# Kernel optimization log

Hardware: AMD Instinct MI355X
Metric: run time of the kernel (lower is better)

Reference implementation:

```python
import jax, jax.numpy as jnp
import numpy as np

DIM = 1024
D_STATE = 16
D_CONV = 4
EXPAND = 2
D_INNER = EXPAND * DIM          # 2048
DT_RANK = DIM // 16             # 64 (ceil(1024/16))
BATCH = 4096
LN_EPS = 1e-5


def setup_inputs() -> dict:
    key = jax.random.key(0)
    ks = jax.random.split(key, 8)
    s = lambda k, shape, sc=0.02: (jax.random.normal(k, shape, jnp.float32) * sc)
    return {
        "x": jax.random.normal(ks[0], (BATCH, DIM), jnp.float32),
        "ln_gamma": jnp.ones((DIM,), jnp.float32),
        "ln_beta": jnp.zeros((DIM,), jnp.float32),
        "W_in": s(ks[1], (2 * D_INNER, DIM)),            # in_proj (no bias)
        "conv_w": s(ks[2], (D_INNER, D_CONV), 0.2),      # depthwise causal conv
        "conv_b": jnp.zeros((D_INNER,), jnp.float32),
        "W_xproj": s(ks[3], (DT_RANK + 2 * D_STATE, D_INNER)),
        "W_dt": s(ks[4], (D_INNER, DT_RANK), 0.1),
        "b_dt": s(ks[5], (D_INNER,), 0.5),
        "A_log": jnp.log(jnp.broadcast_to(
            jnp.arange(1, D_STATE + 1, dtype=jnp.float32), (D_INNER, D_STATE))),
        "Dskip": jnp.ones((D_INNER,), jnp.float32),
        "W_out": s(ks[6], (DIM, D_INNER)),               # out_proj (no bias)
    }


def _mamba_layer(x, ln_gamma, ln_beta, W_in, conv_w, conv_b,
                 W_xproj, W_dt, b_dt, A_log, Dskip, W_out):
    # x: [B, dim] -> unsqueeze(1): [B, L=1, dim]
    xs = x[:, None, :]
    # LayerNorm over last dim
    mu = jnp.mean(xs, axis=-1, keepdims=True)
    var = jnp.var(xs, axis=-1, keepdims=True)
    xn = (xs - mu) * jax.lax.rsqrt(var + LN_EPS) * ln_gamma + ln_beta
    # in_proj -> split into x, z   [B, L, d_inner] each
    xz = jnp.einsum('bld,ed->ble', xn, W_in)
    xi, z = jnp.split(xz, 2, axis=-1)
    L = xi.shape[1]
    # depthwise causal conv1d (kernel d_conv, left pad d_conv-1)
    xp = jnp.pad(xi, ((0, 0), (D_CONV - 1, 0), (0, 0)))
    xc = conv_b + sum(conv_w[:, k] * xp[:, k:k + L, :] for k in range(D_CONV))
    xc = jax.nn.silu(xc)
    # x_proj -> dt, B, C
    xdb = jnp.einsum('bld,ed->ble', xc, W_xproj)
    dt, Bm, Cm = jnp.split(xdb, [DT_RANK, DT_RANK + D_STATE], axis=-1)
    dt = jax.nn.softplus(jnp.einsum('blr,dr->bld', dt, W_dt) + b_dt)  # [B,L,d_inner]
    A = -jnp.exp(A_log)                                              # [d_inner,d_state]
    dA = jnp.exp(dt[..., None] * A)                                  # [B,L,d_inner,d_state]
    dBu = dt[..., None] * Bm[:, :, None, :] * xc[..., None]          # [B,L,d_inner,d_state]

    def step(h, inp):
        dA_l, dBu_l, C_l = inp
        h = dA_l * h + dBu_l                    # [B,d_inner,d_state]
        y = jnp.einsum('bdn,bn->bd', h, C_l)    # [B,d_inner]
        return h, y

    h0 = jnp.zeros((x.shape[0], D_INNER, D_STATE), x.dtype)
    _, ys = jax.lax.scan(step, h0, (dA.swapaxes(0, 1), dBu.swapaxes(0, 1), Cm.swapaxes(0, 1)))
    y = ys.swapaxes(0, 1) + Dskip * xc          # [B,L,d_inner]
    y = y * jax.nn.silu(z)
    out = jnp.einsum('ble,de->bld', y, W_out)   # [B,L,dim]
    return out[:, 0, :]                          # squeeze(1)


def reference(x, ln_gamma, ln_beta, W_in, conv_w, conv_b,
              W_xproj, W_dt, b_dt, A_log, Dskip, W_out):
    return _mamba_layer(x, ln_gamma, ln_beta, W_in, conv_w, conv_b,
                        W_xproj, W_dt, b_dt, A_log, Dskip, W_out)
```

## Files before the change

### kernel.cpp

```cpp
#include <hip/hip_runtime.h>
#include <hip/hip_bf16.h>
#include <stdint.h>

#define DIM     1024
#define DINNER  2048
#define BATCH   4096
#define LN_EPS  1e-5f

typedef unsigned short u16;
using f32x4  = __attribute__((ext_vector_type(4))) float;
using bf16x8 = __attribute__((ext_vector_type(8))) __bf16;

__device__ __forceinline__ float bf2f(u16 h) {
    union { unsigned u; float f; } v; v.u = ((unsigned)h) << 16; return v.f;
}
__device__ __forceinline__ u16 f2bf(float f) {
    union { float f; unsigned u; } v; v.f = f;
    unsigned r = v.u + 0x7fffu + ((v.u >> 16) & 1u);
    return (u16)(r >> 16);
}
__device__ __forceinline__ float silu_f(float x) {
    return x / (1.f + __expf(-x));
}

#define AS1 __attribute__((address_space(1)))
#define AS3 __attribute__((address_space(3)))

__device__ __forceinline__ unsigned lds_u32(const void* p) {
    return (unsigned)(unsigned long long)(const AS3 void*)p;
}

__global__ __launch_bounds__(256)
void cvt_ln(const float* __restrict__ x, const float* __restrict__ gamma,
            const float* __restrict__ beta, u16* __restrict__ xn,
            const float4* __restrict__ s0, ushort4* __restrict__ d0, int n0,
            const float4* __restrict__ s1, ushort4* __restrict__ d1, int n1,
            const float4* __restrict__ s2, ushort4* __restrict__ d2, int n2,
            const float4* __restrict__ s3, ushort4* __restrict__ d3, int n3)
{
    const int t = threadIdx.x;
    if (blockIdx.x < BATCH) {
        const int row = blockIdx.x;
        float4 v = ((const float4*)(x + (size_t)row * DIM))[t];
        float s1v = v.x + v.y + v.z + v.w;
        float s2v = v.x*v.x + v.y*v.y + v.z*v.z + v.w*v.w;
        #pragma unroll
        for (int o = 32; o > 0; o >>= 1) {
            s1v += __shfl_down(s1v, o);
            s2v += __shfl_down(s2v, o);
        }
        __shared__ float red[8];
        __shared__ float mv[2];
        const int w = t >> 6, l = t & 63;
        if (l == 0) { red[w] = s1v; red[4 + w] = s2v; }
        __syncthreads();
        if (t == 0) {
            float a = red[0] + red[1] + red[2] + red[3];
            float b = red[4] + red[5] + red[6] + red[7];
            float mu = a * (1.f / DIM);
            float var = b * (1.f / DIM) - mu * mu;
            mv[0] = mu; mv[1] = rsqrtf(var + LN_EPS);
        }
        __syncthreads();
        const float mu = mv[0], rs = mv[1];
        float4 g  = ((const float4*)gamma)[t];
        float4 be = ((const float4*)beta)[t];
        ushort4 o = make_ushort4(
            f2bf((v.x - mu) * rs * g.x + be.x),
            f2bf((v.y - mu) * rs * g.y + be.y),
            f2bf((v.z - mu) * rs * g.z + be.z),
            f2bf((v.w - mu) * rs * g.w + be.w));
        *(ushort4*)(xn + (size_t)row * DIM + t * 4) = o;
    } else {
        int i = (blockIdx.x - BATCH) * 256 + t;
        const int stride = (gridDim.x - BATCH) * 256;
        const int total = n0 + n1 + n2 + n3;
        for (; i < total; i += stride) {
            int j = i; const float4* s; ushort4* d;
            if (j < n0) { s = s0; d = d0; }
            else { j -= n0;
                if (j < n1) { s = s1; d = d1; }
                else { j -= n1;
                    if (j < n2) { s = s2; d = d2; }
                    else { j -= n2; s = s3; d = d3; }
                }
            }
            float4 v = s[j];
            d[j] = make_ushort4(f2bf(v.x), f2bf(v.y), f2bf(v.z), f2bf(v.w));
        }
    }
}

#define DSR(d, adr, OFFSTR) \
    asm volatile("ds_read_b128 %0, %1 offset:" OFFSTR : "=v"(d) : "v"(adr))
#define RD_A8(DST, A0, A1, S0, S1, S2, S3) do { \
    DSR(DST[0][0], A0, S0); DSR(DST[0][1], A1, S0); \
    DSR(DST[1][0], A0, S1); DSR(DST[1][1], A1, S1); \
    DSR(DST[2][0], A0, S2); DSR(DST[2][1], A1, S2); \
    DSR(DST[3][0], A0, S3); DSR(DST[3][1], A1, S3); } while (0)
#define RD_B4(DST, A0, A1, S0, S1) do { \
    DSR(DST[0][0], A0, S0); DSR(DST[0][1], A1, S0); \
    DSR(DST[1][0], A0, S1); DSR(DST[1][1], A1, S1); } while (0)

#define BC8(x) __builtin_bit_cast(bf16x8, x)
#define MF1(C, Av, Bv) C = __builtin_amdgcn_mfma_f32_16x16x32_bf16(BC8(Av), BC8(Bv), C, 0, 0, 0)

#define CL32_LO do { \
    _Pragma("unroll") for (int m = 0; m < 4; ++m) \
    _Pragma("unroll") for (int n = 0; n < 2; ++n) \
    _Pragma("unroll") for (int k = 0; k < 2; ++k) { \
        MF1(acc[m][n],     aLo[m][k], bC0[n][k]); \
        MF1(acc[m][n + 2], aLo[m][k], bC1[n][k]); } } while (0)
#define CL16_HI0 do { \
    _Pragma("unroll") for (int m = 0; m < 4; ++m) \
    _Pragma("unroll") for (int n = 0; n < 2; ++n) \
    _Pragma("unroll") for (int k = 0; k < 2; ++k) \
        MF1(acc[4 + m][n], aHi[m][k], bC0[n][k]); } while (0)
#define CL16_HI1 do { \
    _Pragma("unroll") for (int m = 0; m < 4; ++m) \
    _Pragma("unroll") for (int n = 0; n < 2; ++n) \
    _Pragma("unroll") for (int k = 0; k < 2; ++k) \
        MF1(acc[4 + m][n + 2], aHi[m][k], bC1[n][k]); } while (0)

#define WAIT_LGKM8 do { asm volatile("s_waitcnt lgkmcnt(8)" ::: "memory"); \
    __builtin_amdgcn_sched_barrier(0); } while (0)
#define WAIT_LGKM0 do { asm volatile("s_waitcnt lgkmcnt(0)" ::: "memory"); \
    __builtin_amdgcn_sched_barrier(0); } while (0)

#define TILE_BODY(CA0, CA1, NA0, NA1, NB0, NB1, SDA0, SDA1, SDB0, SDB1, KT) do { \
    RD_A8(aHi, CA0, CA1, "8192", "10240", "12288", "14336"); \
    WAIT_LGKM8; \
    __builtin_amdgcn_s_setprio(1); CL32_LO; __builtin_amdgcn_s_setprio(0); \
    WAIT_LGKM0; \
    asm volatile("s_waitcnt vmcnt(0)" ::: "memory"); \
    __builtin_amdgcn_s_barrier(); \
    stage(SDB0, Bb, KT); stage(SDB1, BbH, KT); \
    stage(SDA0, Ab, KT); stage(SDA1, AbH, KT); \
    __builtin_amdgcn_s_setprio(1); CL16_HI0; __builtin_amdgcn_s_setprio(0); \
    RD_B4(bC0, NB0, NB1, "0", "2048"); \
    RD_A8(aLo, NA0, NA1, "0", "2048", "4096", "6144"); \
    __builtin_amdgcn_s_setprio(1); CL16_HI1; __builtin_amdgcn_s_setprio(0); \
    RD_B4(bC1, NB0, NB1, "4096", "6144"); \
} while (0)

__global__ __launch_bounds__(512, 2)
void gemmP(const u16* __restrict__ A, const u16* __restrict__ B,
           int N, int K, int nkt,
           u16* __restrict__ dst0, u16* __restrict__ dst1,
           const float* __restrict__ conv_w, const float* __restrict__ conv_b)
{
    __shared__ __align__(16) u16 lds[2][4][8192];
    const int tid = threadIdx.x;
    const int wid = tid >> 6, l = tid & 63;
    const int wm = wid >> 2, wn = wid & 3;
    const int lr = l & 15, l16 = l >> 4;
    const int brow = blockIdx.y * 256, bcol = blockIdx.x * 256;

    const int sr = tid >> 3;
    const int skk = ((tid & 7) ^ (sr & 7)) * 8;
    const u16* Ab  = A + (size_t)(brow + sr) * K + skk;
    const u16* Bb  = B + (size_t)(bcol + sr) * K + skk;
    const u16* AbH = Ab + (size_t)128 * K;
    const u16* BbH = Bb + (size_t)128 * K;

    u16* const dA0h0 = &lds[0][0][tid * 8]; u16* const dA0h1 = &lds[0][1][tid * 8];
    u16* const dA1h0 = &lds[1][0][tid * 8]; u16* const dA1h1 = &lds[1][1][tid * 8];
    u16* const dB0h0 = &lds[0][2][tid * 8]; u16* const dB0h1 = &lds[0][3][tid * 8];
    u16* const dB1h0 = &lds[1][2][tid * 8]; u16* const dB1h1 = &lds[1][3][tid * 8];

    const unsigned cxb0 = (unsigned)(((0 + l16) ^ (l & 7)) * 16);
    const unsigned cxb1 = (unsigned)(((4 + l16) ^ (l & 7)) * 16);
    const unsigned aB0 = lds_u32(&lds[0][wm][0]) + (unsigned)(lr * 128);
    const unsigned bB0 = lds_u32(&lds[0][2 + (wn >> 1)][0]) + (unsigned)((wn & 1) * 8192 + lr * 128);
    const unsigned adA00 = aB0 + cxb0, adA01 = aB0 + cxb1;
    const unsigned adA10 = adA00 + 65536, adA11 = adA01 + 65536;
    const unsigned adB00 = bB0 + cxb0, adB01 = bB0 + cxb1;
    const unsigned adB10 = adB00 + 65536, adB11 = adB01 + 65536;

    f32x4 acc[8][4] = {};
    float4 aLo[4][2], aHi[4][2], bC0[2][2], bC1[2][2];

    auto stage = [&](u16* dst, const u16* srcrow, int kt) {
        const u16* s = srcrow + (size_t)kt * 64;
        __builtin_amdgcn_global_load_lds((const AS1 void*)s, (AS3 void*)dst, 16, 0, 0);
        __builtin_amdgcn_global_load_lds((const AS1 void*)(s + (size_t)64 * K),
                                         (AS3 void*)(dst + 4096), 16, 0, 0);
    };

    stage(dB0h0, Bb, 0);  stage(dB0h1, BbH, 0);
    stage(dA0h0, Ab, 0);  stage(dA0h1, AbH, 0);
    stage(dB1h0, Bb, 1);  stage(dB1h1, BbH, 1);
    stage(dA1h0, Ab, 1);  stage(dA1h1, AbH, 1);
    asm volatile("s_waitcnt vmcnt(8)" ::: "memory");
    __builtin_amdgcn_s_barrier();
    RD_B4(bC0, adB00, adB01, "0", "2048");
    RD_B4(bC1, adB00, adB01, "4096", "6144");
    RD_A8(aLo, adA00, adA01, "0", "2048", "4096", "6144");

    const int niter = nkt >> 1;
    for (int i = 0; i < niter; ++i) {
        const int T = 2 * i;
        const int k2 = (T + 2 < nkt) ? T + 2 : nkt - 1;
        const int k3 = (T + 3 < nkt) ? T + 3 : nkt - 1;
        TILE_BODY(adA00, adA01, adA10, adA11, adB10, adB11,
                  dA0h0, dA0h1, dB0h0, dB0h1, k2);
        TILE_BODY(adA10, adA11, adA00, adA01, adB00, adB01,
                  dA1h0, dA1h1, dB1h0, dB1h1, k3);
    }

    asm volatile("s_waitcnt vmcnt(0) lgkmcnt(0)" ::: "memory");
    __builtin_amdgcn_s_barrier();

    float cb[4], cw[4];
    const bool isxc = (bcol < DINNER);
    if (isxc) {
        #pragma unroll
        for (int n = 0; n < 4; ++n) {
            const int cg = bcol + wn * 64 + n * 16 + lr;
            cb[n] = conv_b[cg]; cw[n] = conv_w[cg * 4 + 3];
        }
    }
    u16* eb = &lds[0][0][0];
    #pragma unroll
    for (int m = 0; m < 8; ++m)
        #pragma unroll
        for (int n = 0; n < 4; ++n)
            #pragma unroll
            for (int r = 0; r < 4; ++r) {
                const int rl = wm * 128 + m * 16 + l16 * 4 + r;
                const int cl = wn * 64 + n * 16 + lr;
                float v = acc[m][n][r];
                v = isxc ? silu_f(cb[n] + cw[n] * v) : silu_f(v);
                eb[rl * 256 + (cl ^ (((rl >> 2) & 3) << 4))] = f2bf(v);
            }
    __syncthreads();

    u16* base = isxc ? (dst0 + bcol) : (dst1 + (bcol - DINNER));
    #pragma unroll
    for (int it = 0; it < 16; ++it) {
        const int idx = it * 4096 + tid * 8;
        const int r = idx >> 8, c = idx & 255;
        uint4 v = *(const uint4*)(eb + r * 256 + (c ^ (((r >> 2) & 3) << 4)));
        *(uint4*)(base + (size_t)(brow + r) * DINNER + c) = v;
    }
}

__global__ __launch_bounds__(256)
void gemm_xdb(const u16* __restrict__ xcb, const u16* __restrict__ Wx,
              u16* __restrict__ dtb, float* __restrict__ sbuf)
{
    __shared__ __align__(16) u16 slc[4][2][7168];
    const int t = threadIdx.x, w = t >> 6, l = t & 63;
    const int lr = l & 15, l16 = l >> 4;
    const int brow = blockIdx.x * 16;
    const int wk = w * 512;

    auto stageX = [&](u16* dst, int step) {
        #pragma unroll
        for (int i = 0; i < 2; ++i) {
            const int o = i * 512 + l * 8;
            const int row = o >> 6;
            const int c8 = ((o >> 3) & 7) ^ (row & 7);
            __builtin_amdgcn_global_load_lds(
                (const AS1 void*)(xcb + (size_t)(brow + row) * DINNER + wk + step * 64 + c8 * 8),
                (AS3 void*)(dst + o), 16, 0, 0);
        }
    };
    auto stageW = [&](u16* dst, int step) {
        #pragma unroll
        for (int i = 0; i < 12; ++i) {
            const int o = i * 512 + l * 8;
            const int row = o >> 6;
            const int c8 = ((o >> 3) & 7) ^ (row & 7);
            __builtin_amdgcn_global_load_lds(
                (const AS1 void*)(Wx + (size_t)row * DINNER + wk + step * 64 + c8 * 8),
                (AS3 void*)(dst + 1024 + o), 16, 0, 0);
        }
    };

    f32x4 acc[6] = {};

    stageX(&slc[w][0][0], 0); stageW(&slc[w][0][0], 0);
    stageX(&slc[w][1][0], 1); stageW(&slc[w][1][0], 1);
    asm volatile("s_waitcnt vmcnt(14)" ::: "memory");
    __builtin_amdgcn_sched_barrier(0);

    for (int s = 0; s < 8; ++s) {
        const u16* sl = &slc[w][s & 1][0];
        #pragma unroll
        for (int kk = 0; kk < 2; ++kk) {
            bf16x8 av = *(const bf16x8*)(sl + lr * 64 + (((kk * 4 + l16) ^ (lr & 7)) * 8));
            #pragma unroll
            for (int n = 0; n < 6; ++n) {
                const int rb = n * 16 + lr;
                bf16x8 bv = *(const bf16x8*)(sl + 1024 + rb * 64 + (((kk * 4 + l16) ^ (rb & 7)) * 8));
                acc[n] = __builtin_amdgcn_mfma_f32_16x16x32_bf16(av, bv, acc[n], 0, 0, 0);
            }
        }
        __builtin_amdgcn_sched_barrier(0);
        const int s2 = (s + 2 < 8) ? s + 2 : 7;
        u16* dst = &slc[w][s & 1][0];
        stageX(dst, s2); stageW(dst, s2);
        asm volatile("s_waitcnt vmcnt(14)" ::: "memory");
        __builtin_amdgcn_sched_barrier(0);
    }

    asm volatile("s_waitcnt vmcnt(0)" ::: "memory");
    __syncthreads();

    float* red = (float*)&slc[0][0][0];
    #pragma unroll
    for (int n = 0; n < 6; ++n)
        #pragma unroll
        for (int r = 0; r < 4; ++r)
            red[w * 1536 + (l16 * 4 + r) * 96 + n * 16 + lr] = acc[n][r];
    __syncthreads();
    #pragma unroll
    for (int i = 0; i < 6; ++i) {
        const int idx = i * 256 + t;
        float v = red[idx] + red[1536 + idx] + red[3072 + idx] + red[4608 + idx];
        red[idx] = v;
        const int row = idx / 96, col = idx - row * 96;
        if (col < 64) dtb[(size_t)(brow + row) * 64 + col] = f2bf(v);
    }
    __syncthreads();
    if (t < 16) {
        float s = 0.f;
        #pragma unroll
        for (int n = 0; n < 16; ++n)
            s += red[t * 96 + 64 + n] * red[t * 96 + 80 + n];
        sbuf[brow + t] = s;
    }
}

__global__ __launch_bounds__(256)
void gemm_dt_y(const u16* __restrict__ dtb, const u16* __restrict__ Wdt,
               const float* __restrict__ b_dt, const float* __restrict__ Dskip,
               const float* __restrict__ sbuf,
               const u16* __restrict__ xcb, const u16* __restrict__ szb,
               u16* __restrict__ y)
{
    __shared__ __align__(16) u16 Ds[64 * 64];
    __shared__ __align__(16) u16 Ws[128 * 64];
    __shared__ __align__(16) u16 dts[64 * 128];
    const int t = threadIdx.x, w = t >> 6, l = t & 63;
    const int wr = w >> 1, wc = w & 1;
    const int brow = blockIdx.y * 64;
    const int bcol = blockIdx.x * 128;
    const int lr = l & 15, l16 = l >> 4;
    const int skk = ((l & 7) ^ (l >> 3)) * 8;

    {
        const u16* Dbase = dtb + (size_t)(brow + (l >> 3)) * 64 + skk;
        const u16* Wbase = Wdt + (size_t)(bcol + (l >> 3)) * 64 + skk;
        #pragma unroll
        for (int c = 0; c < 2; ++c) {
            const int seg = c * 4 + w;
            __builtin_amdgcn_global_load_lds(
                (const AS1 void*)(Dbase + (size_t)seg * 8 * 64),
                (AS3 void*)(&Ds[seg * 512]), 16, 0, 0);
        }
        #pragma unroll
        for (int c = 0; c < 4; ++c) {
            const int seg = c * 4 + w;
            __builtin_amdgcn_global_load_lds(
                (const AS1 void*)(Wbase + (size_t)seg * 8 * 64),
                (AS3 void*)(&Ws[seg * 512]), 16, 0, 0);
        }
    }
    __syncthreads();

    f32x4 acc[2][4] = {};
    #pragma unroll
    for (int kk = 0; kk < 2; ++kk) {
        bf16x8 av[2], bv[4];
        #pragma unroll
        for (int m = 0; m < 2; ++m) {
            const int r = wr * 32 + m * 16 + lr;
            av[m] = *(const bf16x8*)(&Ds[r * 64 + (((kk * 4 + l16) ^ (r & 7)) * 8)]);
        }
        #pragma unroll
        for (int n = 0; n < 4; ++n) {
            const int r = wc * 64 + n * 16 + lr;
            bv[n] = *(const bf16x8*)(&Ws[r * 64 + (((kk * 4 + l16) ^ (r & 7)) * 8)]);
        }
        #pragma unroll
        for (int m = 0; m < 2; ++m)
            #pragma unroll
            for (int n = 0; n < 4; ++n)
                acc[m][n] = __builtin_amdgcn_mfma_f32_16x16x32_bf16(av[m], bv[n], acc[m][n], 0, 0, 0);
    }

    #pragma unroll
    for (int m = 0; m < 2; ++m)
        #pragma unroll
        for (int n = 0; n < 4; ++n)
            #pragma unroll
            for (int r = 0; r < 4; ++r) {
                const int row = wr * 32 + m * 16 + l16 * 4 + r;
                const int col = wc * 64 + n * 16 + lr;
                float v = acc[m][n][r] + b_dt[bcol + col];
                float dt = (v > 20.f) ? v : log1pf(__expf(v));
                dts[row * 128 + (col ^ ((row & 7) << 4))] = f2bf(dt);
            }
    __syncthreads();

    const int rlo = t >> 4;
    const int cg  = (t & 15) * 8;
    #pragma unroll
    for (int rr = 0; rr < 4; ++rr) {
        const int row = rr * 16 + rlo;
        const int grow = brow + row;
        const float sr = sbuf[grow];
        uint4 dv = *(const uint4*)(&dts[row * 128 + ((cg ^ ((row & 7) << 4)))]);
        uint4 xv = *(const uint4*)(xcb + (size_t)grow * DINNER + bcol + cg);
        uint4 zv = *(const uint4*)(szb + (size_t)grow * DINNER + bcol + cg);
        float4 D0 = *(const float4*)(Dskip + bcol + cg);
        float4 D1 = *(const float4*)(Dskip + bcol + cg + 4);
        const float* Dp = &D0.x;
        uint4 ov;
        unsigned* op = (unsigned*)&ov;
        #pragma unroll
        for (int k = 0; k < 4; ++k) {
            unsigned du = ((const unsigned*)&dv)[k];
            unsigned xu = ((const unsigned*)&xv)[k];
            unsigned zu = ((const unsigned*)&zv)[k];
            float Da = (k < 2) ? Dp[2 * k]     : (&D1.x)[2 * (k - 2)];
            float Db = (k < 2) ? Dp[2 * k + 1] : (&D1.x)[2 * (k - 2) + 1];
            float y0 = (bf2f((u16)du) * sr + Da) * bf2f((u16)xu) * bf2f((u16)zu);
            float y1 = (bf2f((u16)(du >> 16)) * sr + Db) * bf2f((u16)(xu >> 16)) * bf2f((u16)(zu >> 16));
            op[k] = (unsigned)f2bf(y0) | ((unsigned)f2bf(y1) << 16);
        }
        *(uint4*)(y + (size_t)grow * DINNER + bcol + cg) = ov;
    }
}

__global__ __launch_bounds__(256, 2)
void gemm4n(const u16* __restrict__ A, const u16* __restrict__ Bm,
            float* __restrict__ out)
{
    __shared__ __align__(16) u16 lds[2][12288];
    const int t = threadIdx.x, w = t >> 6, l = t & 63;
    const int wr = w >> 1, wc = w & 1;
    const int lr = l & 15, l16 = l >> 4;

    const int lin = blockIdx.y * 8 + blockIdx.x;
    const int xcd = lin & 7, q = lin >> 3;
    const int by = xcd * 8 + (q >> 3);
    const int bx = q & 7;
    const int brow = by * 64, bcol = bx * 128;
    const int K = DINNER, nkt = 32;

    auto stage = [&](int buf, int kt) {
        #pragma unroll
        for (int c = 0; c < 2; ++c) {
            const int o = c * 256 + t;
            const int sr = o >> 3;
            const int sc = (o & 7) ^ (sr & 7);
            __builtin_amdgcn_global_load_lds(
                (const AS1 void*)(A + (size_t)(brow + sr) * K + kt * 64 + sc * 8),
                (AS3 void*)(&lds[buf][o * 8]), 16, 0, 0);
        }
        #pragma unroll
        for (int c = 0; c < 4; ++c) {
            const int o = c * 256 + t;
            const int sr = o >> 3;
            const int sc = (o & 7) ^ (sr & 7);
            __builtin_amdgcn_global_load_lds(
                (const AS1 void*)(Bm + (size_t)(bcol + sr) * K + kt * 64 + sc * 8),
                (AS3 void*)(&lds[buf][4096 + o * 8]), 16, 0, 0);
        }
    };

    f32x4 acc[2][4] = {};

    stage(0, 0);
    stage(1, 1);
    asm volatile("s_waitcnt vmcnt(6)" ::: "memory");
    __builtin_amdgcn_s_barrier();

    for (int kt = 0; kt < nkt; ++kt) {
        const int cur = kt & 1;
        #pragma unroll
        for (int kk = 0; kk < 2; ++kk) {
            bf16x8 af[2], bf[4];
            #pragma unroll
            for (int m = 0; m < 2; ++m) {
                const int r = wr * 32 + m * 16 + lr;
                af[m] = *(const bf16x8*)(&lds[cur][r * 64 + (((kk * 4 + l16) ^ (r & 7)) * 8)]);
            }
            #pragma unroll
            for (int n = 0; n < 4; ++n) {
                const int r = wc * 64 + n * 16 + lr;
                bf[n] = *(const bf16x8*)(&lds[cur][4096 + r * 64 + (((kk * 4 + l16) ^ (r & 7)) * 8)]);
            }
            #pragma unroll
            for (int m = 0; m < 2; ++m)
                #pragma unroll
                for (int n = 0; n < 4; ++n)
                    acc[m][n] = __builtin_amdgcn_mfma_f32_16x16x32_bf16(af[m], bf[n], acc[m][n], 0, 0, 0);
        }
        __builtin_amdgcn_sched_barrier(0);
        __builtin_amdgcn_s_barrier();
        const int t2 = (kt + 2 < nkt) ? kt + 2 : nkt - 1;
        stage(cur, t2);
        asm volatile("s_waitcnt vmcnt(6)" ::: "memory");
        __builtin_amdgcn_sched_barrier(0);
        __builtin_amdgcn_s_barrier();
    }

    asm volatile("s_waitcnt vmcnt(0) lgkmcnt(0)" ::: "memory");
    __builtin_amdgcn_s_barrier();

    float* eb = (float*)&lds[0][0];
    #pragma unroll
    for (int m = 0; m < 2; ++m)
        #pragma unroll
        for (int n = 0; n < 4; ++n)
            #pragma unroll
            for (int r = 0; r < 4; ++r) {
                const int row = wr * 32 + m * 16 + l16 * 4 + r;
                const int col = wc * 64 + n * 16 + lr;
                eb[row * 128 + (col ^ ((row & 7) << 2))] = acc[m][n][r];
            }
    __syncthreads();
    #pragma unroll
    for (int it = 0; it < 8; ++it) {
        const int idx = it * 1024 + t * 4;
        const int row = idx >> 7, col = idx & 127;
        float4 v = *(const float4*)(eb + row * 128 + ((col ^ ((row & 7) << 2))));
        *(float4*)(out + (size_t)(brow + row) * DIM + bcol + col) = v;
    }
}

extern "C" void kernel_launch(void* const* d_in, const int* in_sizes, int n_in,
                              void* d_out, int out_size, void* d_ws, size_t ws_size,
                              hipStream_t stream) {
    const float* x      = (const float*)d_in[0];
    const float* ln_g   = (const float*)d_in[1];
    const float* ln_b   = (const float*)d_in[2];
    const float* W_in   = (const float*)d_in[3];
    const float* conv_w = (const float*)d_in[4];
    const float* conv_b = (const float*)d_in[5];
    const float* W_xp   = (const float*)d_in[6];
    const float* W_dt   = (const float*)d_in[7];
    const float* b_dt   = (const float*)d_in[8];
    const float* Dskip  = (const float*)d_in[10];
    const float* W_out  = (const float*)d_in[11];
    float* out = (float*)d_out;

    char* ws = (char*)d_ws;
    const size_t MB = 1u << 20;
    u16*  W_in_b  = (u16*)(ws);
    u16*  xn      = (u16*)(ws + 8 * MB);
    u16*  xcb     = (u16*)(ws + 16 * MB);
    u16*  szb     = (u16*)(ws + 32 * MB);
    u16*  W_xp_b  = (u16*)(ws + 55 * MB);
    u16*  W_dt_b  = (u16*)(ws + 56 * MB);
    u16*  dtb     = (u16*)(ws + 57 * MB);
    float* sbuf   = (float*)(ws + 58 * MB);
    u16*  W_out_b = (u16*)(ws + 64 * MB);
    u16*  yb      = (u16*)(ws + 68 * MB);

    cvt_ln<<<BATCH + 2048, 256, 0, stream>>>(
        x, ln_g, ln_b, xn,
        (const float4*)W_in,  (ushort4*)W_in_b,  (2 * DINNER * DIM) / 4,
        (const float4*)W_out, (ushort4*)W_out_b, (DIM * DINNER) / 4,
        (const float4*)W_xp,  (ushort4*)W_xp_b,  (96 * DINNER) / 4,
        (const float4*)W_dt,  (ushort4*)W_dt_b,  (DINNER * 64) / 4);

    gemmP<<<dim3(4096 / 256, BATCH / 256, 1), 512, 0, stream>>>(
        xn, W_in_b, 4096, DIM, DIM / 64, xcb, szb, conv_w, conv_b);

    gemm_xdb<<<BATCH / 16, 256, 0, stream>>>(xcb, W_xp_b, dtb, sbuf);

    gemm_dt_y<<<dim3(DINNER / 128, BATCH / 64), 256, 0, stream>>>(
        dtb, W_dt_b, b_dt, Dskip, sbuf, xcb, szb, yb);

    gemm4n<<<dim3(DIM / 128, BATCH / 64), 256, 0, stream>>>(yb, W_out_b, out);
}
```

Before: 119.4 us.

## Fuse x_proj and dt_proj/y-gating kernels into one per-row-block kernel

```diff
diff --git a/kernel.cpp b/kernel.cpp
--- a/kernel.cpp
+++ b/kernel.cpp
@@ -246,10 +246,16 @@
 }
 
 __global__ __launch_bounds__(256)
-void gemm_xdb(const u16* __restrict__ xcb, const u16* __restrict__ Wx,
-              u16* __restrict__ dtb, float* __restrict__ sbuf)
+void xdb_dty(const u16* __restrict__ xcb, const u16* __restrict__ Wx,
+             const u16* __restrict__ Wdt,
+             const float* __restrict__ b_dt, const float* __restrict__ Dskip,
+             const u16* __restrict__ szb, u16* __restrict__ yb)
 {
     __shared__ __align__(16) u16 slc[4][2][7168];
+    u16* const lbase = &slc[0][0][0];
+    float* const red = (float*)lbase;
+    u16*  const dta  = lbase + 12288;
+    float* const sS  = (float*)(lbase + 13312);
     const int t = threadIdx.x, w = t >> 6, l = t & 63;
     const int lr = l & 15, l16 = l >> 4;
     const int brow = blockIdx.x * 16;
@@ -308,7 +314,6 @@
     asm volatile("s_waitcnt vmcnt(0)" ::: "memory");
     __syncthreads();
 
-    float* red = (float*)&slc[0][0][0];
     #pragma unroll
     for (int n = 0; n < 6; ++n)
         #pragma unroll
@@ -321,7 +326,8 @@
         float v = red[idx] + red[1536 + idx] + red[3072 + idx] + red[4608 + idx];
         red[idx] = v;
         const int row = idx / 96, col = idx - row * 96;
-        if (col < 64) dtb[(size_t)(brow + row) * 64 + col] = f2bf(v);
+        if (col < 64)
+            dta[row * 64 + (((col >> 3) ^ (row & 7)) * 8) + (col & 7)] = f2bf(v);
     }
     __syncthreads();
     if (t < 16) {
@@ -329,109 +335,101 @@
         #pragma unroll
         for (int n = 0; n < 16; ++n)
             s += red[t * 96 + 64 + n] * red[t * 96 + 80 + n];
-        sbuf[brow + t] = s;
-    }
-}
-
-__global__ __launch_bounds__(256)
-void gemm_dt_y(const u16* __restrict__ dtb, const u16* __restrict__ Wdt,
-               const float* __restrict__ b_dt, const float* __restrict__ Dskip,
-               const float* __restrict__ sbuf,
-               const u16* __restrict__ xcb, const u16* __restrict__ szb,
-               u16* __restrict__ y)
-{
-    __shared__ __align__(16) u16 Ds[64 * 64];
-    __shared__ __align__(16) u16 Ws[128 * 64];
-    __shared__ __align__(16) u16 dts[64 * 128];
-    const int t = threadIdx.x, w = t >> 6, l = t & 63;
-    const int wr = w >> 1, wc = w & 1;
-    const int brow = blockIdx.y * 64;
-    const int bcol = blockIdx.x * 128;
-    const int lr = l & 15, l16 = l >> 4;
-    const int skk = ((l & 7) ^ (l >> 3)) * 8;
-
-    {
-        const u16* Dbase = dtb + (size_t)(brow + (l >> 3)) * 64 + skk;
-        const u16* Wbase = Wdt + (size_t)(bcol + (l >> 3)) * 64 + skk;
-        #pragma unroll
-        for (int c = 0; c < 2; ++c) {
-            const int seg = c * 4 + w;
+        sS[t] = s;
+    }
+    __syncthreads();
+
+    const int cg0 = w * 512;
+    u16* const wdtw = lbase + 16384 + w * 8192;
+    u16* const dttw = lbase + 49152 + w * 1024;
+
+    auto stageD = [&](u16* dst, int g) {
+        #pragma unroll
+        for (int i = 0; i < 8; ++i) {
+            const int o = i * 512 + l * 8;
+            const int row = o >> 6;
+            const int c8 = ((o >> 3) & 7) ^ (row & 7);
             __builtin_amdgcn_global_load_lds(
-                (const AS1 void*)(Dbase + (size_t)seg * 8 * 64),
-                (AS3 void*)(&Ds[seg * 512]), 16, 0, 0);
-        }
-        #pragma unroll
-        for (int c = 0; c < 4; ++c) {
-            const int seg = c * 4 + w;
-            __builtin_amdgcn_global_load_lds(
-                (const AS1 void*)(Wbase + (size_t)seg * 8 * 64),
-                (AS3 void*)(&Ws[seg * 512]), 16, 0, 0);
-        }
-    }
-    __syncthreads();
-
-    f32x4 acc[2][4] = {};
-    #pragma unroll
-    for (int kk = 0; kk < 2; ++kk) {
-        bf16x8 av[2], bv[4];
-        #pragma unroll
-        for (int m = 0; m < 2; ++m) {
-            const int r = wr * 32 + m * 16 + lr;
-            av[m] = *(const bf16x8*)(&Ds[r * 64 + (((kk * 4 + l16) ^ (r & 7)) * 8)]);
-        }
-        #pragma unroll
-        for (int n = 0; n < 4; ++n) {
-            const int r = wc * 64 + n * 16 + lr;
-            bv[n] = *(const bf16x8*)(&Ws[r * 64 + (((kk * 4 + l16) ^ (r & 7)) * 8)]);
-        }
-        #pragma unroll
-        for (int m = 0; m < 2; ++m)
-            #pragma unroll
-            for (int n = 0; n < 4; ++n)
-                acc[m][n] = __builtin_amdgcn_mfma_f32_16x16x32_bf16(av[m], bv[n], acc[m][n], 0, 0, 0);
-    }
-
-    #pragma unroll
-    for (int m = 0; m < 2; ++m)
+                (const AS1 void*)(Wdt + (size_t)(cg0 + g * 64 + row) * 64 + c8 * 8),
+                (AS3 void*)(dst + o), 16, 0, 0);
+        }
+    };
+
+    float bdt[8][4];
+    #pragma unroll
+    for (int g = 0; g < 8; ++g)
         #pragma unroll
         for (int n = 0; n < 4; ++n)
+            bdt[g][n] = b_dt[cg0 + g * 64 + n * 16 + lr];
+
+    stageD(wdtw, 0);
+    stageD(wdtw + 4096, 1);
+    asm volatile("s_waitcnt vmcnt(8)" ::: "memory");
+    __builtin_amdgcn_sched_barrier(0);
+
+    bf16x8 aA[2];
+    #pragma unroll
+    for (int kk = 0; kk < 2; ++kk)
+        aA[kk] = *(const bf16x8*)(dta + lr * 64 + (((kk * 4 + l16) ^ (lr & 7)) * 8));
+
+    for (int g = 0; g < 8; ++g) {
+        __builtin_amdgcn_sched_barrier(0);
+        const u16* cw = wdtw + (g & 1) * 4096;
+        f32x4 acc2[4] = {};
+        #pragma unroll
+        for (int kk = 0; kk < 2; ++kk)
+            #pragma unroll
+            for (int n = 0; n < 4; ++n) {
+                const int rb = n * 16 + lr;
+                bf16x8 bv = *(const bf16x8*)(cw + rb * 64 + (((kk * 4 + l16) ^ (rb & 7)) * 8));
+                acc2[n] = __builtin_amdgcn_mfma_f32_16x16x32_bf16(aA[kk], bv, acc2[n], 0, 0, 0);
+            }
+        #pragma unroll
+        for (int n = 0; n < 4; ++n)
             #pragma unroll
             for (int r = 0; r < 4; ++r) {
-                const int row = wr * 32 + m * 16 + l16 * 4 + r;
-                const int col = wc * 64 + n * 16 + lr;
-                float v = acc[m][n][r] + b_dt[bcol + col];
+                const int row = l16 * 4 + r;
+                const int col = n * 16 + lr;
+                float v = acc2[n][r] + bdt[g][n];
                 float dt = (v > 20.f) ? v : log1pf(__expf(v));
-                dts[row * 128 + (col ^ ((row & 7) << 4))] = f2bf(dt);
-            }
-    __syncthreads();
-
-    const int rlo = t >> 4;
-    const int cg  = (t & 15) * 8;
-    #pragma unroll
-    for (int rr = 0; rr < 4; ++rr) {
-        const int row = rr * 16 + rlo;
-        const int grow = brow + row;
-        const float sr = sbuf[grow];
-        uint4 dv = *(const uint4*)(&dts[row * 128 + ((cg ^ ((row & 7) << 4)))]);
-        uint4 xv = *(const uint4*)(xcb + (size_t)grow * DINNER + bcol + cg);
-        uint4 zv = *(const uint4*)(szb + (size_t)grow * DINNER + bcol + cg);
-        float4 D0 = *(const float4*)(Dskip + bcol + cg);
-        float4 D1 = *(const float4*)(Dskip + bcol + cg + 4);
-        const float* Dp = &D0.x;
-        uint4 ov;
-        unsigned* op = (unsigned*)&ov;
-        #pragma unroll
-        for (int k = 0; k < 4; ++k) {
-            unsigned du = ((const unsigned*)&dv)[k];
-            unsigned xu = ((const unsigned*)&xv)[k];
-            unsigned zu = ((const unsigned*)&zv)[k];
-            float Da = (k < 2) ? Dp[2 * k]     : (&D1.x)[2 * (k - 2)];
-            float Db = (k < 2) ? Dp[2 * k + 1] : (&D1.x)[2 * (k - 2) + 1];
-            float y0 = (bf2f((u16)du) * sr + Da) * bf2f((u16)xu) * bf2f((u16)zu);
-            float y1 = (bf2f((u16)(du >> 16)) * sr + Db) * bf2f((u16)(xu >> 16)) * bf2f((u16)(zu >> 16));
-            op[k] = (unsigned)f2bf(y0) | ((unsigned)f2bf(y1) << 16);
-        }
-        *(uint4*)(y + (size_t)grow * DINNER + bcol + cg) = ov;
+                dttw[row * 64 + (col ^ ((row & 7) << 3))] = f2bf(dt);
+            }
+        const int gcol = cg0 + g * 64 + (l & 7) * 8;
+        uint4 xv[2], zv[2];
+        #pragma unroll
+        for (int it = 0; it < 2; ++it) {
+            const int r2 = (l >> 3) + 8 * it;
+            xv[it] = *(const uint4*)(xcb + (size_t)(brow + r2) * DINNER + gcol);
+            zv[it] = *(const uint4*)(szb + (size_t)(brow + r2) * DINNER + gcol);
+        }
+        float4 D0 = *(const float4*)(Dskip + gcol);
+        float4 D1 = *(const float4*)(Dskip + gcol + 4);
+        __builtin_amdgcn_sched_barrier(0);
+        const int g2 = (g + 2 < 8) ? g + 2 : 7;
+        stageD(wdtw + (g & 1) * 4096, g2);
+        asm volatile("s_waitcnt vmcnt(8)" ::: "memory");
+        __builtin_amdgcn_sched_barrier(0);
+        #pragma unroll
+        for (int it = 0; it < 2; ++it) {
+            const int r2 = (l >> 3) + 8 * it;
+            const float sr = sS[r2];
+            uint4 dv = *(const uint4*)(dttw + r2 * 64 + ((((l & 7) ^ (r2 & 7))) * 8));
+            const float* Dp = &D0.x;
+            uint4 ov;
+            unsigned* op = (unsigned*)&ov;
+            #pragma unroll
+            for (int k = 0; k < 4; ++k) {
+                unsigned du = ((const unsigned*)&dv)[k];
+                unsigned xu = ((const unsigned*)&xv[it])[k];
+                unsigned zu = ((const unsigned*)&zv[it])[k];
+                float Da = (k < 2) ? Dp[2 * k]     : (&D1.x)[2 * (k - 2)];
+                float Db = (k < 2) ? Dp[2 * k + 1] : (&D1.x)[2 * (k - 2) + 1];
+                float y0 = (bf2f((u16)du) * sr + Da) * bf2f((u16)xu) * bf2f((u16)zu);
+                float y1 = (bf2f((u16)(du >> 16)) * sr + Db) * bf2f((u16)(xu >> 16)) * bf2f((u16)(zu >> 16));
+                op[k] = (unsigned)f2bf(y0) | ((unsigned)f2bf(y1) << 16);
+            }
+            *(uint4*)(yb + (size_t)(brow + r2) * DINNER + gcol) = ov;
+        }
     }
 }
 
@@ -557,8 +555,6 @@
     u16*  szb     = (u16*)(ws + 32 * MB);
     u16*  W_xp_b  = (u16*)(ws + 55 * MB);
     u16*  W_dt_b  = (u16*)(ws + 56 * MB);
-    u16*  dtb     = (u16*)(ws + 57 * MB);
-    float* sbuf   = (float*)(ws + 58 * MB);
     u16*  W_out_b = (u16*)(ws + 64 * MB);
     u16*  yb      = (u16*)(ws + 68 * MB);
 
@@ -572,10 +568,8 @@
     gemmP<<<dim3(4096 / 256, BATCH / 256, 1), 512, 0, stream>>>(
         xn, W_in_b, 4096, DIM, DIM / 64, xcb, szb, conv_w, conv_b);
 
-    gemm_xdb<<<BATCH / 16, 256, 0, stream>>>(xcb, W_xp_b, dtb, sbuf);
-
-    gemm_dt_y<<<dim3(DINNER / 128, BATCH / 64), 256, 0, stream>>>(
-        dtb, W_dt_b, b_dt, Dskip, sbuf, xcb, szb, yb);
+    xdb_dty<<<BATCH / 16, 256, 0, stream>>>(
+        xcb, W_xp_b, W_dt_b, b_dt, Dskip, szb, yb);
 
     gemm4n<<<dim3(DIM / 128, BATCH / 64), 256, 0, stream>>>(yb, W_out_b, out);
 }
```

Result: slower. 129.2 us (median of 2 runs) (+8.2%).
